# Performance work log

Hardware: AMD Instinct MI355X
Metric: run time of the kernel (lower is better)

Reference implementation:

```python
import jax, jax.numpy as jnp
import numpy as np
from jax import lax

ML = 3      # mL: intermediate channels of the generated smoother
K = 7       # kernelSize of the generated per-sample kernels
HID = 100   # MLP hidden width


def _conv2d(x, w, pad):
    # x: [N,C,H,W], w: [O,I,kh,kw], 'same'-style padding `pad`
    return lax.conv_general_dilated(
        x, w, window_strides=(1, 1), padding=[(pad, pad), (pad, pad)],
        dimension_numbers=('NCHW', 'OIHW', 'NCHW'))


def _batch_conv2d(inputs, kernels, pad=1):
    # grouped conv trick: inputs [B,1,H,W], kernels [B,1,kh,kw] -> [B,1,H,W]
    B, _, H, W = inputs.shape
    out = lax.conv_general_dilated(
        inputs.reshape(1, B, H, W), kernels, window_strides=(1, 1),
        padding=[(pad, pad), (pad, pad)], feature_group_count=B,
        dimension_numbers=('NCHW', 'OIHW', 'NCHW'))
    return out.reshape(B, 1, H, W)


def setup_inputs() -> dict:
    key = jax.random.key(0)
    ks = jax.random.split(key, 11)
    B, N = 32, 1024
    out_dim = ML * K * K
    inp = {
        'x': jax.random.normal(ks[0], (B, 1, N, N), jnp.float32),
        'f': jax.random.normal(ks[1], (B, 1, N, N), jnp.float32),
        'kernelA': jax.random.normal(ks[2], (B, 1, 3, 3), jnp.float32) * 0.5,
        # fc1: Linear(9,100) -> ReLU -> Linear(100, mL*K*K)   (stored [in,out])
        'fc1_w1': jax.random.normal(ks[3], (9, HID), jnp.float32) / np.sqrt(9.0),
        'fc1_b1': jnp.zeros((HID,), jnp.float32),
        'fc1_w2': jax.random.normal(ks[4], (HID, out_dim), jnp.float32) / np.sqrt(HID),
        'fc1_b2': jnp.zeros((out_dim,), jnp.float32),
        'fc2_w1': jax.random.normal(ks[5], (9, HID), jnp.float32) / np.sqrt(9.0),
        'fc2_b1': jnp.zeros((HID,), jnp.float32),
        'fc2_w2': jax.random.normal(ks[6], (HID, out_dim), jnp.float32) / np.sqrt(HID),
        'fc2_b2': jnp.zeros((out_dim,), jnp.float32),
    }
    return inp


def reference(x, f, kernelA, fc1_w1, fc1_b1, fc1_w2, fc1_b2,
              fc2_w1, fc2_b1, fc2_w2, fc2_b2):
    B = x.shape[0]
    pad = K // 2
    w = kernelA.reshape(B, 9)                                  # flatten(kernelA, 1)
    h1 = jax.nn.relu(w @ fc1_w1 + fc1_b1)
    weight1 = (h1 @ fc1_w2 + fc1_b2).reshape(B, ML, 1, K, K)
    h2 = jax.nn.relu(w @ fc2_w1 + fc2_b1)
    weight2 = (h2 @ fc2_w2 + fc2_b2).reshape(B, 1, ML, K, K)

    Ax = _batch_conv2d(x, kernelA, pad=1)
    r = f - Ax                                                 # residual [B,1,N,N]

    def per_sample(ri, w1, w2):
        # ri: [1,N,N]; w1: [mL,1,K,K]; w2: [1,mL,K,K]
        tmp = _conv2d(ri[None], w1, pad)                       # [1,mL,N,N]
        return _conv2d(tmp, w2, pad)[0]                        # [1,N,N]

    G2 = jax.vmap(per_sample)(r, weight1, weight2)             # [B,1,N,N]
    return x + G2
```

## Files before the change

### kernel.cpp

```cpp
#include <hip/hip_runtime.h>

#define N    1024
#define BSZ  32
#define PS   480
#define HID  100

__global__ __launch_bounds__(256) void prep_kernel(
    const float* __restrict__ kernelA,
    const float* __restrict__ fc1_w1, const float* __restrict__ fc1_b1,
    const float* __restrict__ fc1_w2, const float* __restrict__ fc1_b2,
    const float* __restrict__ fc2_w1, const float* __restrict__ fc2_b1,
    const float* __restrict__ fc2_w2, const float* __restrict__ fc2_b2,
    float* __restrict__ params)
{
    int b = blockIdx.x, t = threadIdx.x;
    __shared__ float w[9], h1[HID], h2[HID], w1[147], w2[147];
    if (t < 9) w[t] = kernelA[b * 9 + t];
    __syncthreads();
    if (t < HID) {
        float s1 = fc1_b1[t], s2 = fc2_b1[t];
        #pragma unroll
        for (int i = 0; i < 9; ++i) {
            s1 = fmaf(w[i], fc1_w1[i * HID + t], s1);
            s2 = fmaf(w[i], fc2_w1[i * HID + t], s2);
        }
        h1[t] = fmaxf(s1, 0.f);
        h2[t] = fmaxf(s2, 0.f);
    }
    __syncthreads();
    if (t < 147) {
        float s1 = fc1_b2[t], s2 = fc2_b2[t];
        for (int i = 0; i < HID; ++i) {
            s1 = fmaf(h1[i], fc1_w2[i * 147 + t], s1);
            s2 = fmaf(h2[i], fc2_w2[i * 147 + t], s2);
        }
        w1[t] = s1;
        w2[t] = s2;
    }
    __syncthreads();
    float* P = params + b * PS;
    if (t < 169) {
        int ey = t / 13, ex = t % 13;
        float s = 0.f;
        for (int m = 0; m < 3; ++m)
            for (int d1y = 0; d1y < 7; ++d1y) {
                int d2y = ey - d1y;
                if (d2y < 0 || d2y > 6) continue;
                for (int d1x = 0; d1x < 7; ++d1x) {
                    int d2x = ex - d1x;
                    if (d2x < 0 || d2x > 6) continue;
                    s = fmaf(w1[m * 49 + d1y * 7 + d1x],
                             w2[m * 49 + d2y * 7 + d2x], s);
                }
            }
        P[t] = s;
    }
    if (t < 147) { P[169 + t] = w1[t]; P[316 + t] = w2[t]; }
    if (t < 9)   P[463 + t] = w[t];
}

#define TR 32
#define TC 128
#define XR 46
#define XC 144
#define RRW 44
#define RC 140
#define NQ 1540

__device__ __forceinline__ void conv_row(const float* win, const float* __restrict__ P,
                                         int ky, float* accRow)
{
    #pragma unroll
    for (int c = 0; c < 13; ++c) {
        float tv = P[ky * 13 + c];
        #pragma unroll
        for (int j = 0; j < 4; ++j)
            accRow[j] = fmaf(win[c + j], tv, accRow[j]);
    }
}

__global__ __launch_bounds__(256, 6) void main_kernel(
    const float* __restrict__ X, const float* __restrict__ F,
    const float* __restrict__ params, float* __restrict__ out)
{
    __shared__ __align__(16) float buf[XR * XC];
    const int t  = threadIdx.x;
    const int b  = blockIdx.z;
    const int y0 = blockIdx.y * TR;
    const int x0 = blockIdx.x * TC;
    const float* P  = params + b * PS;
    const float* Xb = X + (size_t)b * N * N;
    const float* Fb = F + (size_t)b * N * N;
    float*       Ob = out + (size_t)b * N * N;

    for (int idx = t; idx < XR * XC; idx += 256) {
        int i = idx / XC, j = idx - i * XC;
        int gy = y0 - 7 + i, gx = x0 - 7 + j;
        buf[idx] = (gy >= 0 && gy < N && gx >= 0 && gx < N) ? Xb[gy * N + gx] : 0.f;
    }
    __syncthreads();

    float ka[9];
    #pragma unroll
    for (int i = 0; i < 9; ++i) ka[i] = P[463 + i];

    float rq[7][4];
    #pragma unroll
    for (int k = 0; k < 7; ++k) {
        int idx = t + k * 256;
        if (idx < NQ) {
            int i = idx / 35;
            int j = (idx - i * 35) * 4;
            const float* xr = &buf[i * XC + j];
            float s[4] = {0.f, 0.f, 0.f, 0.f};
            #pragma unroll
            for (int dy = 0; dy < 3; ++dy) {
                float w8[8];
                float4 v0 = *reinterpret_cast<const float4*>(xr + dy * XC);
                float4 v1 = *reinterpret_cast<const float4*>(xr + dy * XC + 4);
                w8[0] = v0.x; w8[1] = v0.y; w8[2] = v0.z; w8[3] = v0.w;
                w8[4] = v1.x; w8[5] = v1.y; w8[6] = v1.z; w8[7] = v1.w;
                #pragma unroll
                for (int dx = 0; dx < 3; ++dx)
                    #pragma unroll
                    for (int c = 0; c < 4; ++c)
                        s[c] = fmaf(ka[dy * 3 + dx], w8[dx + c], s[c]);
            }
            int gy = y0 - 6 + i, gxb = x0 - 6 + j;
            #pragma unroll
            for (int c = 0; c < 4; ++c) {
                int gx = gxb + c;
                float v = 0.f;
                if (gy >= 0 && gy < N && gx >= 0 && gx < N)
                    v = Fb[gy * N + gx] - s[c];
                rq[k][c] = v;
            }
        }
    }
    __syncthreads();

    #pragma unroll
    for (int k = 0; k < 7; ++k) {
        int idx = t + k * 256;
        if (idx < NQ) {
            int i = idx / 35;
            int j = (idx - i * 35) * 4;
            float4 v; v.x = rq[k][0]; v.y = rq[k][1]; v.z = rq[k][2]; v.w = rq[k][3];
            *reinterpret_cast<float4*>(&buf[i * RC + j]) = v;
        }
    }
    __syncthreads();

    const int tx4 = (t & 31) * 4;
    const int ty4 = (t >> 5) * 4;
    const float* rbase = &buf[ty4 * RC + tx4];

    float acc[4][4] = {{0.f,0.f,0.f,0.f},{0.f,0.f,0.f,0.f},
                       {0.f,0.f,0.f,0.f},{0.f,0.f,0.f,0.f}};
    float win[16];

    #define LOAD_WIN(rr)                                                     \
        { float4 v0 = *reinterpret_cast<const float4*>(rbase + (rr) * RC);   \
          float4 v1 = *reinterpret_cast<const float4*>(rbase + (rr) * RC + 4);\
          float4 v2 = *reinterpret_cast<const float4*>(rbase + (rr) * RC + 8);\
          float4 v3 = *reinterpret_cast<const float4*>(rbase + (rr) * RC + 12);\
          win[0]=v0.x; win[1]=v0.y; win[2]=v0.z; win[3]=v0.w;                \
          win[4]=v1.x; win[5]=v1.y; win[6]=v1.z; win[7]=v1.w;                \
          win[8]=v2.x; win[9]=v2.y; win[10]=v2.z; win[11]=v2.w;              \
          win[12]=v3.x; win[13]=v3.y; win[14]=v3.z; win[15]=v3.w; }

    LOAD_WIN(0);
    conv_row(win, P, 0, acc[0]);
    LOAD_WIN(1);
    conv_row(win, P, 1, acc[0]);
    conv_row(win, P, 0, acc[1]);
    LOAD_WIN(2);
    conv_row(win, P, 2, acc[0]);
    conv_row(win, P, 1, acc[1]);
    conv_row(win, P, 0, acc[2]);

    for (int rr = 3; rr <= 12; ++rr) {
        LOAD_WIN(rr);
        #pragma unroll
        for (int i = 0; i < 4; ++i)
            conv_row(win, P, rr - i, acc[i]);
    }

    LOAD_WIN(13);
    conv_row(win, P, 12, acc[1]);
    conv_row(win, P, 11, acc[2]);
    conv_row(win, P, 10, acc[3]);
    LOAD_WIN(14);
    conv_row(win, P, 12, acc[2]);
    conv_row(win, P, 11, acc[3]);
    LOAD_WIN(15);
    conv_row(win, P, 12, acc[3]);

    #pragma unroll
    for (int i = 0; i < 4; ++i) {
        const float4 xq = *reinterpret_cast<const float4*>(
            &Xb[(y0 + ty4 + i) * N + (x0 + tx4)]);
        float4 o;
        o.x = xq.x + acc[i][0]; o.y = xq.y + acc[i][1];
        o.z = xq.z + acc[i][2]; o.w = xq.w + acc[i][3];
        *reinterpret_cast<float4*>(&Ob[(y0 + ty4 + i) * N + (x0 + tx4)]) = o;
    }
}

#define SEG 64
#define AXX 14
#define AXU (SEG + 14)
#define ARR 12
#define ARU (SEG + 12)
#define ATA 6
#define ATU (SEG + 6)

__global__ __launch_bounds__(256) void border_kernel(
    const float* __restrict__ X, const float* __restrict__ F,
    const float* __restrict__ params, float* __restrict__ out)
{
    __shared__ float xs[AXX * AXU];
    __shared__ float rs[ARR * ARU];
    __shared__ float tmp[3 * ATA * ATU];
    __shared__ float sw1[147], sw2[147];

    const int  t    = threadIdx.x;
    const int  b    = blockIdx.y;
    const int  seg  = blockIdx.x;
    const int  edge = seg >> 4;
    const int  s    = seg & 15;
    const bool vert = edge >= 2;
    const bool hi   = (edge == 1) || (edge == 3);
    const int  T0   = hi ? (N - 6) : 0;
    const int  V0   = hi ? (N - 3) : 0;
    const int  D    = hi ? 3 : 0;
    const int  u0   = vert ? (3 + s * SEG) : (s * SEG);
    const int  acr0x = T0 - 4, al0x = u0 - 7;
    const int  acr0r = T0 - 3, al0r = u0 - 6;

    const float* P  = params + b * PS;
    const float* Xb = X + (size_t)b * N * N;
    const float* Fb = F + (size_t)b * N * N;
    float*       Ob = out + (size_t)b * N * N;

    if (t < 147) { sw1[t] = P[169 + t]; sw2[t] = P[316 + t]; }
    float ka[9];
    #pragma unroll
    for (int i = 0; i < 9; ++i) ka[i] = P[463 + i];

    for (int idx = t; idx < AXX * AXU; idx += 256) {
        int a = vert ? (idx % AXX) : (idx / AXU);
        int u = vert ? (idx / AXX) : (idx % AXU);
        int ga = acr0x + a, gl = al0x + u;
        int gy = vert ? gl : ga, gx = vert ? ga : gl;
        xs[a * AXU + u] =
            (gy >= 0 && gy < N && gx >= 0 && gx < N) ? Xb[gy * N + gx] : 0.f;
    }
    __syncthreads();

    for (int idx = t; idx < ARR * ARU; idx += 256) {
        int a = vert ? (idx % ARR) : (idx / ARU);
        int u = vert ? (idx / ARR) : (idx % ARU);
        int ga = acr0r + a, gl = al0r + u;
        int gy = vert ? gl : ga, gx = vert ? ga : gl;
        float v = 0.f;
        if (gy >= 0 && gy < N && gx >= 0 && gx < N) {
            float sc = 0.f;
            #pragma unroll
            for (int da = 0; da < 3; ++da)
                #pragma unroll
                for (int dl = 0; dl < 3; ++dl)
                    sc = fmaf(ka[vert ? (dl * 3 + da) : (da * 3 + dl)],
                              xs[(a + da) * AXU + (u + dl)], sc);
            v = Fb[gy * N + gx] - sc;
        }
        rs[a * ARU + u] = v;
    }
    __syncthreads();

    for (int idx = t; idx < 3 * ATA * ATU; idx += 256) {
        int m   = idx / (ATA * ATU);
        int rem = idx - m * (ATA * ATU);
        int a = rem / ATU, u = rem % ATU;
        int gl = (u0 - 3) + u;
        float sc = 0.f;
        if (gl >= 0 && gl < N) {
            #pragma unroll
            for (int da = 0; da < 7; ++da)
                #pragma unroll
                for (int dl = 0; dl < 7; ++dl)
                    sc = fmaf(sw1[m * 49 + (vert ? (dl * 7 + da) : (da * 7 + dl))],
                              rs[(a + da) * ARU + (u + dl)], sc);
        }
        tmp[idx] = sc;
    }
    __syncthreads();

    for (int idx = t; idx < 3 * SEG; idx += 256) {
        int v = idx / SEG, u = idx - (idx / SEG) * SEG;
        int gl = u0 + u, ga = V0 + v;
        if (vert && gl >= N - 3) continue;
        float sc = 0.f;
        #pragma unroll
        for (int m = 0; m < 3; ++m)
            #pragma unroll
            for (int d2a = 0; d2a < 7; ++d2a) {
                int aT = v + d2a - 3 + D;
                if (aT < 0 || aT >= ATA) continue;
                #pragma unroll
                for (int d2l = 0; d2l < 7; ++d2l)
                    sc = fmaf(sw2[m * 49 + (vert ? (d2l * 7 + d2a) : (d2a * 7 + d2l))],
                              tmp[(m * ATA + aT) * ATU + (u + d2l)], sc);
            }
        int gy = vert ? gl : ga, gx = vert ? ga : gl;
        float xv = xs[(ga - acr0x) * AXU + (gl - al0x)];
        Ob[gy * N + gx] = xv + sc;
    }
}

extern "C" void kernel_launch(void* const* d_in, const int* in_sizes, int n_in,
                              void* d_out, int out_size, void* d_ws, size_t ws_size,
                              hipStream_t stream)
{
    const float* x    = (const float*)d_in[0];
    const float* f    = (const float*)d_in[1];
    const float* kA   = (const float*)d_in[2];
    const float* f1w1 = (const float*)d_in[3];
    const float* f1b1 = (const float*)d_in[4];
    const float* f1w2 = (const float*)d_in[5];
    const float* f1b2 = (const float*)d_in[6];
    const float* f2w1 = (const float*)d_in[7];
    const float* f2b1 = (const float*)d_in[8];
    const float* f2w2 = (const float*)d_in[9];
    const float* f2b2 = (const float*)d_in[10];
    float* out    = (float*)d_out;
    float* params = (float*)d_ws;

    prep_kernel<<<BSZ, 256, 0, stream>>>(kA, f1w1, f1b1, f1w2, f1b2,
                                         f2w1, f2b1, f2w2, f2b2, params);
    main_kernel<<<dim3(N / TC, N / TR, BSZ), 256, 0, stream>>>(x, f, params, out);
    border_kernel<<<dim3(64, BSZ), 256, 0, stream>>>(x, f, params, out);
}
```

Before: 542.7 us.

## Replace border recompute with atomic correction kernel and prefetch F/X loads

The border kernel, which recomputed the edge outputs from scratch, is replaced by a correction kernel. It subtracts from the main kernel's output the contribution of the intermediate tmp values that lie outside the image (the main kernel does not zero them), using atomicAdd on the output. The main kernel also issues its F loads early, before the first barrier, and loads the X values for the final add before the convolution loop, so global latency overlaps with compute. The correction kernel works on a thinner strip with wider segments but adds atomics, and it relies on the main kernel's exact border behaviour. Corner regions may be corrected twice.

```diff
diff --git a/kernel.cpp b/kernel.cpp
--- a/kernel.cpp
+++ b/kernel.cpp
@@ -98,6 +98,31 @@
         int gy = y0 - 7 + i, gx = x0 - 7 + j;
         buf[idx] = (gy >= 0 && gy < N && gx >= 0 && gx < N) ? Xb[gy * N + gx] : 0.f;
     }
+
+    float fq[7][4];
+    #pragma unroll
+    for (int k = 0; k < 7; ++k) {
+        int idx = t + k * 256;
+        fq[k][0] = fq[k][1] = fq[k][2] = fq[k][3] = 0.f;
+        if (idx < NQ) {
+            int i = idx / 35;
+            int j = (idx - i * 35) * 4;
+            int gy = y0 - 6 + i, gxb = x0 - 6 + j;
+            if (gy >= 0 && gy < N) {
+                if (gxb >= 0 && gxb + 3 < N) {
+                    float2 a = *reinterpret_cast<const float2*>(&Fb[gy * N + gxb]);
+                    float2 c = *reinterpret_cast<const float2*>(&Fb[gy * N + gxb + 2]);
+                    fq[k][0] = a.x; fq[k][1] = a.y; fq[k][2] = c.x; fq[k][3] = c.y;
+                } else {
+                    #pragma unroll
+                    for (int c = 0; c < 4; ++c) {
+                        int gx = gxb + c;
+                        if (gx >= 0 && gx < N) fq[k][c] = Fb[gy * N + gx];
+                    }
+                }
+            }
+        }
+    }
     __syncthreads();
 
     float ka[9];
@@ -130,10 +155,8 @@
             #pragma unroll
             for (int c = 0; c < 4; ++c) {
                 int gx = gxb + c;
-                float v = 0.f;
-                if (gy >= 0 && gy < N && gx >= 0 && gx < N)
-                    v = Fb[gy * N + gx] - s[c];
-                rq[k][c] = v;
+                rq[k][c] = (gy >= 0 && gy < N && gx >= 0 && gx < N)
+                           ? (fq[k][c] - s[c]) : 0.f;
             }
         }
     }
@@ -154,6 +177,11 @@
     const int tx4 = (t & 31) * 4;
     const int ty4 = (t >> 5) * 4;
     const float* rbase = &buf[ty4 * RC + tx4];
+
+    float4 xq[4];
+    #pragma unroll
+    for (int i = 0; i < 4; ++i)
+        xq[i] = *reinterpret_cast<const float4*>(&Xb[(y0 + ty4 + i) * N + (x0 + tx4)]);
 
     float acc[4][4] = {{0.f,0.f,0.f,0.f},{0.f,0.f,0.f,0.f},
                        {0.f,0.f,0.f,0.f},{0.f,0.f,0.f,0.f}};
@@ -198,45 +226,37 @@
 
     #pragma unroll
     for (int i = 0; i < 4; ++i) {
-        const float4 xq = *reinterpret_cast<const float4*>(
-            &Xb[(y0 + ty4 + i) * N + (x0 + tx4)]);
         float4 o;
-        o.x = xq.x + acc[i][0]; o.y = xq.y + acc[i][1];
-        o.z = xq.z + acc[i][2]; o.w = xq.w + acc[i][3];
+        o.x = xq[i].x + acc[i][0]; o.y = xq[i].y + acc[i][1];
+        o.z = xq[i].z + acc[i][2]; o.w = xq[i].w + acc[i][3];
         *reinterpret_cast<float4*>(&Ob[(y0 + ty4 + i) * N + (x0 + tx4)]) = o;
     }
 }
 
-#define SEG 64
-#define AXX 14
-#define AXU (SEG + 14)
-#define ARR 12
-#define ARU (SEG + 12)
-#define ATA 6
-#define ATU (SEG + 6)
-
-__global__ __launch_bounds__(256) void border_kernel(
+#define CSEG   256
+#define TEX_U  262
+#define TPITCH 264
+#define REX_U  268
+#define RPITCH 272
+#define XEX_U  270
+#define XPITCH 272
+
+__global__ __launch_bounds__(256) void corr_kernel(
     const float* __restrict__ X, const float* __restrict__ F,
     const float* __restrict__ params, float* __restrict__ out)
 {
-    __shared__ float xs[AXX * AXU];
-    __shared__ float rs[ARR * ARU];
-    __shared__ float tmp[3 * ATA * ATU];
+    __shared__ float xs[5 * XPITCH];
+    __shared__ float rs[3 * RPITCH];
+    __shared__ float tmp[9 * TPITCH];
     __shared__ float sw1[147], sw2[147];
 
     const int  t    = threadIdx.x;
-    const int  b    = blockIdx.y;
-    const int  seg  = blockIdx.x;
-    const int  edge = seg >> 4;
-    const int  s    = seg & 15;
-    const bool vert = edge >= 2;
-    const bool hi   = (edge == 1) || (edge == 3);
-    const int  T0   = hi ? (N - 6) : 0;
-    const int  V0   = hi ? (N - 3) : 0;
-    const int  D    = hi ? 3 : 0;
-    const int  u0   = vert ? (3 + s * SEG) : (s * SEG);
-    const int  acr0x = T0 - 4, al0x = u0 - 7;
-    const int  acr0r = T0 - 3, al0r = u0 - 6;
+    const int  b    = blockIdx.z;
+    const int  edge = blockIdx.y;
+    const int  u0   = blockIdx.x * CSEG;
+    const bool vert = (edge >= 2);
+    const bool hi   = (edge & 1);
+    const int  ar0  = hi ? (N - 3) : 0;
 
     const float* P  = params + b * PS;
     const float* Xb = X + (size_t)b * N * N;
@@ -248,20 +268,18 @@
     #pragma unroll
     for (int i = 0; i < 9; ++i) ka[i] = P[463 + i];
 
-    for (int idx = t; idx < AXX * AXU; idx += 256) {
-        int a = vert ? (idx % AXX) : (idx / AXU);
-        int u = vert ? (idx / AXX) : (idx % AXU);
-        int ga = acr0x + a, gl = al0x + u;
+    for (int idx = t; idx < 5 * XEX_U; idx += 256) {
+        int ax = idx / XEX_U, u = idx - ax * XEX_U;
+        int ga = (ar0 - 1) + ax, gl = u0 - 7 + u;
         int gy = vert ? gl : ga, gx = vert ? ga : gl;
-        xs[a * AXU + u] =
+        xs[ax * XPITCH + u] =
             (gy >= 0 && gy < N && gx >= 0 && gx < N) ? Xb[gy * N + gx] : 0.f;
     }
     __syncthreads();
 
-    for (int idx = t; idx < ARR * ARU; idx += 256) {
-        int a = vert ? (idx % ARR) : (idx / ARU);
-        int u = vert ? (idx / ARR) : (idx % ARU);
-        int ga = acr0r + a, gl = al0r + u;
+    for (int idx = t; idx < 3 * REX_U; idx += 256) {
+        int ar = idx / REX_U, u = idx - ar * REX_U;
+        int ga = ar0 + ar, gl = u0 - 6 + u;
         int gy = vert ? gl : ga, gx = vert ? ga : gl;
         float v = 0.f;
         if (gy >= 0 && gy < N && gx >= 0 && gx < N) {
@@ -271,50 +289,53 @@
                 #pragma unroll
                 for (int dl = 0; dl < 3; ++dl)
                     sc = fmaf(ka[vert ? (dl * 3 + da) : (da * 3 + dl)],
-                              xs[(a + da) * AXU + (u + dl)], sc);
+                              xs[(ar + da) * XPITCH + (u + dl)], sc);
             v = Fb[gy * N + gx] - sc;
         }
-        rs[a * ARU + u] = v;
-    }
-    __syncthreads();
-
-    for (int idx = t; idx < 3 * ATA * ATU; idx += 256) {
-        int m   = idx / (ATA * ATU);
-        int rem = idx - m * (ATA * ATU);
-        int a = rem / ATU, u = rem % ATU;
-        int gl = (u0 - 3) + u;
+        rs[ar * RPITCH + u] = v;
+    }
+    __syncthreads();
+
+    for (int idx = t; idx < 9 * TEX_U; idx += 256) {
+        int m   = idx / (3 * TEX_U);
+        int rem = idx - m * (3 * TEX_U);
+        int ai = rem / TEX_U, u = rem - ai * TEX_U;
+        int bl = u0 - 3 + u;
         float sc = 0.f;
-        if (gl >= 0 && gl < N) {
-            #pragma unroll
-            for (int da = 0; da < 7; ++da)
+        if (!vert || (bl >= 0 && bl < N)) {
+            #pragma unroll
+            for (int da = 0; da < 7; ++da) {
+                int ri = hi ? (ai + da) : (ai - 6 + da);
+                if (ri < 0 || ri > 2) continue;
                 #pragma unroll
                 for (int dl = 0; dl < 7; ++dl)
                     sc = fmaf(sw1[m * 49 + (vert ? (dl * 7 + da) : (da * 7 + dl))],
-                              rs[(a + da) * ARU + (u + dl)], sc);
-        }
-        tmp[idx] = sc;
-    }
-    __syncthreads();
-
-    for (int idx = t; idx < 3 * SEG; idx += 256) {
-        int v = idx / SEG, u = idx - (idx / SEG) * SEG;
-        int gl = u0 + u, ga = V0 + v;
-        if (vert && gl >= N - 3) continue;
-        float sc = 0.f;
+                              rs[ri * RPITCH + (u + dl)], sc);
+            }
+        }
+        tmp[(m * 3 + ai) * TPITCH + u] = sc;
+    }
+    __syncthreads();
+
+    for (int idx = t; idx < 3 * CSEG; idx += 256) {
+        int oy = idx / CSEG, u = idx - oy * CSEG;
+        int ol = u0 + u;
+        int oa = hi ? (N - 3 + oy) : oy;
+        float C = 0.f;
         #pragma unroll
         for (int m = 0; m < 3; ++m)
             #pragma unroll
-            for (int d2a = 0; d2a < 7; ++d2a) {
-                int aT = v + d2a - 3 + D;
-                if (aT < 0 || aT >= ATA) continue;
+            for (int ai = 0; ai < 3; ++ai) {
+                int dperp = hi ? (ai - oy + 6) : (ai - oy);
+                if (dperp < 0 || dperp > 6) continue;
                 #pragma unroll
-                for (int d2l = 0; d2l < 7; ++d2l)
-                    sc = fmaf(sw2[m * 49 + (vert ? (d2l * 7 + d2a) : (d2a * 7 + d2l))],
-                              tmp[(m * ATA + aT) * ATU + (u + d2l)], sc);
-            }
-        int gy = vert ? gl : ga, gx = vert ? ga : gl;
-        float xv = xs[(ga - acr0x) * AXU + (gl - al0x)];
-        Ob[gy * N + gx] = xv + sc;
+                for (int du = 0; du < 7; ++du)
+                    C = fmaf(sw2[m * 49 + (vert ? (du * 7 + dperp)
+                                                : (dperp * 7 + du))],
+                             tmp[(m * 3 + ai) * TPITCH + (u + du)], C);
+            }
+        int gy = vert ? ol : oa, gx = vert ? oa : ol;
+        atomicAdd(&Ob[gy * N + gx], -C);
     }
 }
 
@@ -339,5 +360,5 @@
     prep_kernel<<<BSZ, 256, 0, stream>>>(kA, f1w1, f1b1, f1w2, f1b2,
                                          f2w1, f2b1, f2w2, f2b2, params);
     main_kernel<<<dim3(N / TC, N / TR, BSZ), 256, 0, stream>>>(x, f, params, out);
-    border_kernel<<<dim3(64, BSZ), 256, 0, stream>>>(x, f, params, out);
-}
+    corr_kernel<<<dim3(N / CSEG, 4, BSZ), 256, 0, stream>>>(x, f, params, out);
+}
```

New measurement: 698.9 us. 1.29x slower.
